# Optimization experiments

Hardware: AMD Instinct MI355X
Metric: run time of the kernel (lower is better)

## Reference

```python
import jax, jax.numpy as jnp
import numpy as np

B, T, S, D = 4, 16, 256, 1024
H, HKV = 16, 4
HD = D // H  # 64
N_IMG = 240  # image tokens; remaining S-N_IMG are agent tokens
LOGIT_CAP = 50.0
EPS = 1e-6


def _build_mask():
    # modality-aware mask: image tokens see only image tokens; agent tokens see all
    m = np.zeros((S, S), dtype=bool)
    m[:N_IMG, :N_IMG] = True
    m[N_IMG:, :] = True
    return jnp.asarray(m)


def _build_rope(s, hd):
    half = hd // 2
    inv_freq = 1.0 / (10000.0 ** (np.arange(half, dtype=np.float32) / half))
    pos = np.arange(s, dtype=np.float32)
    ang = np.outer(pos, inv_freq)  # (S, hd/2)
    return jnp.asarray(np.cos(ang)), jnp.asarray(np.sin(ang))


def setup_inputs() -> dict:
    key = jax.random.key(0)
    ks = jax.random.split(key, 7)
    rope_cos, rope_sin = _build_rope(S, HD)
    sc = 0.02
    return {
        "x": jax.random.normal(ks[0], (B, T, S, D), jnp.float32),
        "attn_mask": _build_mask(),
        "rope_cos": rope_cos,
        "rope_sin": rope_sin,
        "Wq": jax.random.normal(ks[1], (D, H * HD), jnp.float32) * sc,
        "Wk": jax.random.normal(ks[2], (D, HKV * HD), jnp.float32) * sc,
        "Wv": jax.random.normal(ks[3], (D, HKV * HD), jnp.float32) * sc,
        "Wo": jax.random.normal(ks[4], (D, D), jnp.float32) * sc,
        "q_scale": jnp.ones((HD,), jnp.float32),
        "k_scale": jnp.ones((HD,), jnp.float32),
    }


def _rmsnorm(t, scale):
    # RMSNorm over head_dim
    var = jnp.mean(jnp.square(t), axis=-1, keepdims=True)
    return t * jax.lax.rsqrt(var + EPS) * scale


def _rope(t, cos, sin):
    # rotate-half RoPE; t: (N, S, h, hd), cos/sin: (S, hd/2)
    half = t.shape[-1] // 2
    t1, t2 = t[..., :half], t[..., half:]
    c = cos[None, :, None, :]
    s = sin[None, :, None, :]
    return jnp.concatenate([t1 * c - t2 * s, t2 * c + t1 * s], axis=-1)


def reference(x, attn_mask, rope_cos, rope_sin, Wq, Wk, Wv, Wo, q_scale, k_scale):
    b, t, s, d = x.shape
    n = b * t
    xf = x.reshape(n, s, d)
    q = (xf @ Wq).reshape(n, s, H, HD)
    k = (xf @ Wk).reshape(n, s, HKV, HD)
    v = (xf @ Wv).reshape(n, s, HKV, HD)
    # QK-norm then RoPE
    q = _rope(_rmsnorm(q, q_scale), rope_cos, rope_sin)
    k = _rope(_rmsnorm(k, k_scale), rope_cos, rope_sin)
    # GQA: repeat kv heads
    rep = H // HKV
    k = jnp.repeat(k, rep, axis=2)
    v = jnp.repeat(v, rep, axis=2)
    scale = 1.0 / jnp.sqrt(jnp.asarray(HD, x.dtype))
    scores = jnp.einsum('nqhd,nkhd->nhqk', q, k) * scale
    # logit soft-capping
    scores = LOGIT_CAP * jnp.tanh(scores / LOGIT_CAP)
    big_neg = jnp.asarray(jnp.finfo(scores.dtype).min, scores.dtype)
    scores = jnp.where(attn_mask[None, None], scores, big_neg)
    p = jax.nn.softmax(scores, axis=-1)
    out = jnp.einsum('nhqk,nkhd->nqhd', p, v).reshape(n, s, d)
    return (out @ Wo).reshape(b, t, s, d)
```

## Files before the change

kernel.cpp:

```cpp
#include <hip/hip_runtime.h>

typedef __bf16 v8bf __attribute__((ext_vector_type(8)));
typedef __bf16 v4bf __attribute__((ext_vector_type(4)));
typedef float floatx4 __attribute__((ext_vector_type(4)));

#define MFMA16(a, b, c) __builtin_amdgcn_mfma_f32_16x16x32_bf16(a, b, c, 0, 0, 0)
#define GLL16(gp, lp)                                                        \
    __builtin_amdgcn_global_load_lds(                                        \
        (const __attribute__((address_space(1))) void*)(gp),                 \
        (__attribute__((address_space(3))) void*)(lp), 16, 0, 0)

__global__ void cast_x(const float* __restrict__ x, __bf16* __restrict__ xb, int n4) {
    int i = blockIdx.x * blockDim.x + threadIdx.x;
    int stride = gridDim.x * blockDim.x;
    for (; i < n4; i += stride) {
        float4 v = ((const float4*)x)[i];
        v4bf o;
        o[0] = (__bf16)v.x; o[1] = (__bf16)v.y; o[2] = (__bf16)v.z; o[3] = (__bf16)v.w;
        ((v4bf*)xb)[i] = o;
    }
}

__global__ void transW(const float* __restrict__ W0, const float* __restrict__ W1,
                       const float* __restrict__ W2, const float* __restrict__ W3,
                       __bf16* __restrict__ dqkv, __bf16* __restrict__ dwo) {
    __shared__ __bf16 tile[64][65];
    int k0 = blockIdx.x * 64;
    int byy = blockIdx.y;
    bool isO = byy >= 24;
    int c0 = (isO ? byy - 24 : byy) * 64;
    for (int i = threadIdx.x; i < 4096; i += 256) {
        int k = i >> 6, c = i & 63;
        int gc = c0 + c;
        float v;
        if (isO)            v = W3[(k0 + k) * 1024 + gc];
        else if (gc < 1024) v = W0[(k0 + k) * 1024 + gc];
        else if (gc < 1280) v = W1[(k0 + k) * 256 + gc - 1024];
        else                v = W2[(k0 + k) * 256 + gc - 1280];
        tile[c][k] = (__bf16)v;
    }
    __syncthreads();
    __bf16* dst = isO ? dwo : dqkv;
    for (int i = threadIdx.x; i < 4096; i += 256) {
        int c = i >> 6, k = i & 63;
        dst[(c0 + c) * 1024 + k0 + k] = tile[c][k];
    }
}

template <typename OUT>
__global__ __launch_bounds__(256) void gemm_bt(const __bf16* __restrict__ A,
                                               const __bf16* __restrict__ B,
                                               OUT* __restrict__ C, int N) {
    __shared__ __attribute__((aligned(16))) __bf16 smem[16384];
    __bf16* As = smem;
    __bf16* Bs = smem + 8192;
    const int t = threadIdx.x, lane = t & 63, w = t >> 6;
    const int m0 = blockIdx.y * 128, n0 = blockIdx.x * 128;
    const int wm = (w >> 1) * 64, wn = (w & 1) * 64;
    const int rl = lane >> 2;
    const int gl = (lane & 3) ^ ((lane >> 3) & 3);
    const __bf16* pA0 = A + (long)(m0 + w * 16 + rl) * 1024 + gl * 8;
    const __bf16* pA1 = A + (long)(m0 + 64 + w * 16 + rl) * 1024 + gl * 8;
    const __bf16* pB0 = B + (long)(n0 + w * 16 + rl) * 1024 + gl * 8;
    const __bf16* pB1 = B + (long)(n0 + 64 + w * 16 + rl) * 1024 + gl * 8;
    __bf16* lA0 = &As[(w * 16) * 32];
    __bf16* lA1 = &As[(64 + w * 16) * 32];
    __bf16* lB0 = &Bs[(w * 16) * 32];
    __bf16* lB1 = &Bs[(64 + w * 16) * 32];
    const int lr = lane & 15, quad = lane >> 4, m = lane & 15;
    const int ga = ((quad ^ ((lr >> 1) & 3)) * 8);
    floatx4 acc[4][4] = {};
    for (int kk = 0; kk < 1024; kk += 64) {
        __syncthreads();
        GLL16(pA0 + kk, lA0);          GLL16(pA0 + kk + 32, lA0 + 4096);
        GLL16(pA1 + kk, lA1);          GLL16(pA1 + kk + 32, lA1 + 4096);
        GLL16(pB0 + kk, lB0);          GLL16(pB0 + kk + 32, lB0 + 4096);
        GLL16(pB1 + kk, lB1);          GLL16(pB1 + kk + 32, lB1 + 4096);
        __syncthreads();
#pragma unroll
        for (int p = 0; p < 2; ++p) {
            v8bf af[4], bq[4];
#pragma unroll
            for (int i = 0; i < 4; ++i)
                af[i] = *(const v8bf*)(&As[p * 4096 + (wm + i * 16 + lr) * 32 + ga]);
#pragma unroll
            for (int j = 0; j < 4; ++j)
                bq[j] = *(const v8bf*)(&Bs[p * 4096 + (wn + j * 16 + lr) * 32 + ga]);
#pragma unroll
            for (int i = 0; i < 4; ++i)
#pragma unroll
                for (int j = 0; j < 4; ++j)
                    acc[i][j] = MFMA16(af[i], bq[j], acc[i][j]);
        }
    }
    __syncthreads();
    const int row2 = lane >> 2, cb = lane & 3;
    if constexpr (sizeof(OUT) == 2) {
        __bf16* tile = smem + w * (16 * 68);
#pragma unroll
        for (int i = 0; i < 4; ++i) {
#pragma unroll
            for (int j = 0; j < 4; ++j)
#pragma unroll
                for (int r = 0; r < 4; ++r)
                    tile[(quad * 4 + r) * 68 + j * 16 + m] = (__bf16)acc[i][j][r];
            __bf16* dst = (__bf16*)C + (long)(m0 + wm + i * 16 + row2) * N + n0 + wn + cb * 16;
            *(v8bf*)dst = *(const v8bf*)(&tile[row2 * 68 + cb * 16]);
            *(v8bf*)(dst + 8) = *(const v8bf*)(&tile[row2 * 68 + cb * 16 + 8]);
        }
    } else {
        float* tile = (float*)smem + w * (16 * 66);
#pragma unroll
        for (int i = 0; i < 4; ++i) {
#pragma unroll
            for (int j = 0; j < 4; ++j)
#pragma unroll
                for (int r = 0; r < 4; ++r)
                    tile[(quad * 4 + r) * 66 + j * 16 + m] = acc[i][j][r];
            float* dst = (float*)C + (long)(m0 + wm + i * 16 + row2) * N + n0 + wn + cb * 16;
#pragma unroll
            for (int c = 0; c < 4; ++c)
                *(floatx4*)(dst + c * 4) = *(const floatx4*)(&tile[row2 * 66 + cb * 16 + c * 4]);
        }
    }
}

__global__ __launch_bounds__(256) void knorm(const __bf16* __restrict__ qkv,
                                             const float* __restrict__ rc,
                                             const float* __restrict__ rs,
                                             const float* __restrict__ ksc,
                                             __bf16* __restrict__ Kb) {
    int item = blockIdx.x * 4 + (threadIdx.x >> 6);
    int lane = threadIdx.x & 63;
    int row = item >> 2, hk = item & 3;
    int n = row >> 8, s = row & 255;
    float v = (float)qkv[(long)row * 1536 + 1024 + hk * 64 + lane];
    float sq = v * v;
#pragma unroll
    for (int msk = 1; msk < 64; msk <<= 1) sq += __shfl_xor(sq, msk);
    float rr = rsqrtf(sq * (1.f / 64.f) + 1e-6f);
    v = v * rr * ksc[lane];
    float c = rc[s * 32 + (lane & 31)];
    float sn = rs[s * 32 + (lane & 31)];
    float p = __shfl_xor(v, 32);
    v = (lane < 32) ? (v * c - p * sn) : (v * c + p * sn);
    Kb[((long)((n * 4 + hk) * 256 + s) << 6) + lane] = (__bf16)v;
}

__global__ __launch_bounds__(512) void attn_kernel(const __bf16* __restrict__ qkv,
                                                   const __bf16* __restrict__ Kb,
                                                   const float* __restrict__ rc,
                                                   const float* __restrict__ rs,
                                                   const float* __restrict__ qsc,
                                                   __bf16* __restrict__ O) {
    __shared__ __attribute__((aligned(16))) __bf16 KV[256 * 64];
    __shared__ __attribute__((aligned(16))) __bf16 Ps[8][16][40];
    const int bx = blockIdx.x;
    const int n = bx >> 5, h = (bx >> 1) & 15, half = bx & 1, hk = h >> 2;
    const int t = threadIdx.x, lane = t & 63, w = t >> 6;
    const int m = lane & 15, quad = lane >> 4;

    for (int p = 0; p < 4; ++p) {
        int l = t + p * 512;
        int s = l >> 3, cg = l & 7;
        v8bf kv = *(const v8bf*)(Kb + ((long)((n * 4 + hk) * 256 + s) << 6) + cg * 8);
        *(v8bf*)(&KV[s * 64 + ((cg ^ (s & 7)) * 8)]) = kv;
    }
    const int srow = half * 128 + w * 16 + m;
    const __bf16* qp = qkv + (long)(n * 256 + srow) * 1536 + h * 64 + quad * 8;
    v8bf qr0 = *(const v8bf*)(qp);
    v8bf qr1 = *(const v8bf*)(qp + 32);
    float f0[8], f1[8], ss = 0.f;
#pragma unroll
    for (int j = 0; j < 8; ++j) {
        f0[j] = (float)qr0[j]; f1[j] = (float)qr1[j];
        ss += f0[j] * f0[j] + f1[j] * f1[j];
    }
    ss += __shfl_xor(ss, 16);
    ss += __shfl_xor(ss, 32);
    float rr = rsqrtf(ss * (1.f / 64.f) + 1e-6f);
    v8bf qa0, qa1;
#pragma unroll
    for (int j = 0; j < 8; ++j) {
        int hd = quad * 8 + j;
        float t1 = f0[j] * rr * qsc[hd];
        float t2 = f1[j] * rr * qsc[32 + hd];
        float c = rc[srow * 32 + hd], sn = rs[srow * 32 + hd];
        qa0[j] = (__bf16)(t1 * c - t2 * sn);
        qa1[j] = (__bf16)(t2 * c + t1 * sn);
    }
    __syncthreads();

    floatx4 sc[16];
#pragma unroll
    for (int ti = 0; ti < 16; ++ti) {
        int kr = ti * 16 + m;
        v8bf b0 = *(const v8bf*)(&KV[kr * 64 + ((quad ^ (kr & 7)) * 8)]);
        v8bf b1 = *(const v8bf*)(&KV[kr * 64 + (((quad + 4) ^ (kr & 7)) * 8)]);
        floatx4 a = {0.f, 0.f, 0.f, 0.f};
        a = MFMA16(qa0, b0, a);
        a = MFMA16(qa1, b1, a);
        sc[ti] = a;
    }

    const int qbase = half * 128 + w * 16 + quad * 4;
    float sum[4] = {0.f, 0.f, 0.f, 0.f};
#pragma unroll
    for (int ti = 0; ti < 16; ++ti)
#pragma unroll
        for (int r = 0; r < 4; ++r) {
            float v = sc[ti][r];
            float e = __builtin_amdgcn_exp2f(v * 0.0072134752f);
            float capped = 50.f - 100.f * __builtin_amdgcn_rcpf(e + 1.f);
            float p = __builtin_amdgcn_exp2f(capped * 1.44269504f);
            if (ti == 15 && (qbase + r) < 240) p = 0.f;
            sc[ti][r] = p;
            sum[r] += p;
        }
    float inv[4];
#pragma unroll
    for (int r = 0; r < 4; ++r) {
#pragma unroll
        for (int msk = 1; msk < 16; msk <<= 1) sum[r] += __shfl_xor(sum[r], msk);
        inv[r] = __builtin_amdgcn_rcpf(sum[r]);
    }

    __syncthreads();
    for (int p = 0; p < 4; ++p) {
        int l = t + p * 512;
        int s = l >> 3, cg = l & 7;
        v8bf vv = *(const v8bf*)(qkv + (long)(n * 256 + s) * 1536 + 1280 + hk * 64 + cg * 8);
#pragma unroll
        for (int j = 0; j < 8; ++j)
            KV[(cg * 8 + j) * 256 + ((s >> 3) ^ j) * 8 + (s & 7)] = vv[j];
    }
    __syncthreads();

    floatx4 oacc[4] = {};
#pragma unroll
    for (int kc = 0; kc < 8; ++kc) {
#pragma unroll
        for (int ht = 0; ht < 2; ++ht) {
            int ti = kc * 2 + ht;
#pragma unroll
            for (int r = 0; r < 4; ++r)
                Ps[w][quad * 4 + r][ht * 16 + m] = (__bf16)sc[ti][r];
        }
        v8bf pa = *(const v8bf*)(&Ps[w][m][quad * 8]);
#pragma unroll
        for (int ct = 0; ct < 4; ++ct) {
            int hd = ct * 16 + m;
            int sg = kc * 4 + quad;
            v8bf vb = *(const v8bf*)(&KV[hd * 256 + ((sg ^ (hd & 7)) * 8)]);
            oacc[ct] = MFMA16(pa, vb, oacc[ct]);
        }
    }
#pragma unroll
    for (int ct = 0; ct < 4; ++ct)
#pragma unroll
        for (int r = 0; r < 4; ++r) {
            int qrow = half * 128 + w * 16 + quad * 4 + r;
            O[(long)(n * 256 + qrow) * 1024 + h * 64 + ct * 16 + m] =
                (__bf16)(oacc[ct][r] * inv[r]);
        }
}

extern "C" void kernel_launch(void* const* d_in, const int* in_sizes, int n_in,
                              void* d_out, int out_size, void* d_ws, size_t ws_size,
                              hipStream_t stream) {
    const float* x  = (const float*)d_in[0];
    const float* rc = (const float*)d_in[2];
    const float* rs = (const float*)d_in[3];
    const float* Wq = (const float*)d_in[4];
    const float* Wk = (const float*)d_in[5];
    const float* Wv = (const float*)d_in[6];
    const float* Wo = (const float*)d_in[7];
    const float* qs = (const float*)d_in[8];
    const float* ks = (const float*)d_in[9];
    float* out = (float*)d_out;
    char* ws = (char*)d_ws;

    __bf16* x_bf    = (__bf16*)(ws);
    __bf16* WqkvT   = (__bf16*)(ws + (32l << 20));
    __bf16* WoT     = (__bf16*)(ws + (35l << 20));
    __bf16* qkv_bf  = (__bf16*)(ws + (37l << 20));
    __bf16* K_bf    = (__bf16*)(ws + (85l << 20));
    __bf16* attn_bf = (__bf16*)(ws + (93l << 20));

    cast_x<<<4096, 256, 0, stream>>>(x, x_bf, 16777216 / 4);
    transW<<<dim3(16, 40), 256, 0, stream>>>(Wq, Wk, Wv, Wo, WqkvT, WoT);
    gemm_bt<__bf16><<<dim3(12, 128), 256, 0, stream>>>(x_bf, WqkvT, qkv_bf, 1536);
    knorm<<<16384, 256, 0, stream>>>(qkv_bf, rc, rs, ks, K_bf);
    attn_kernel<<<2048, 512, 0, stream>>>(qkv_bf, K_bf, rc, rs, qs, attn_bf);
    gemm_bt<float><<<dim3(8, 128), 256, 0, stream>>>(attn_bf, WoT, out, 1024);
}
```

Measured before the change: 331.1 us.

## Pipeline GEMM with 4-stage async LDS ring, larger tiles and grid swizzle

Rewrites the bf16 GEMM so global-to-LDS loads are issued three k-steps ahead into a 4-slot shared-memory ring, synchronised with explicit vmcnt waits and barriers instead of a full sync per step. Tiles grow to 128x256 or 256x256 with 512 threads, and workgroup ids are remapped so neighbouring blocks share operand tiles in cache. MFMA sections are raised in priority with setprio. The larger LDS footprint and tile size may cut occupancy, and the hand-written wait counts must match the issued loads exactly.

Result: no change. 324.7 us (-1.9%).

```diff
diff --git a/kernel.cpp b/kernel.cpp
--- a/kernel.cpp
+++ b/kernel.cpp
@@ -9,6 +9,8 @@
     __builtin_amdgcn_global_load_lds(                                        \
         (const __attribute__((address_space(1))) void*)(gp),                 \
         (__attribute__((address_space(3))) void*)(lp), 16, 0, 0)
+#define VMW(n) asm volatile("s_waitcnt vmcnt(" #n ")" ::: "memory")
+#define BARRIER() asm volatile("s_barrier" ::: "memory")
 
 __global__ void cast_x(const float* __restrict__ x, __bf16* __restrict__ xb, int n4) {
     int i = blockIdx.x * blockDim.x + threadIdx.x;
@@ -47,58 +49,83 @@
     }
 }
 
-template <typename OUT>
-__global__ __launch_bounds__(256) void gemm_bt(const __bf16* __restrict__ A,
-                                               const __bf16* __restrict__ B,
-                                               OUT* __restrict__ C, int N) {
-    __shared__ __attribute__((aligned(16))) __bf16 smem[16384];
-    __bf16* As = smem;
-    __bf16* Bs = smem + 8192;
+template <int BM, typename OUT>
+__global__ __launch_bounds__(512, 2) void gemm_bt(const __bf16* __restrict__ A,
+                                                  const __bf16* __restrict__ B,
+                                                  OUT* __restrict__ C, int N) {
+    constexpr int MF = BM / 32;
+    constexpr int SLAB = (BM + 256) * 32;
+    __shared__ __attribute__((aligned(16))) __bf16 smem[4 * SLAB];
     const int t = threadIdx.x, lane = t & 63, w = t >> 6;
-    const int m0 = blockIdx.y * 128, n0 = blockIdx.x * 128;
-    const int wm = (w >> 1) * 64, wn = (w & 1) * 64;
+    const int gx = gridDim.x;
+    const int nwg = gx * gridDim.y;
+    const int id = blockIdx.y * gx + blockIdx.x;
+    const int swz = (id & 7) * (nwg >> 3) + (id >> 3);
+    const int m0 = (swz / gx) * BM, n0 = (swz % gx) * 256;
+    const int wm = (w >> 2) * (BM / 2), wn = (w & 3) * 64;
     const int rl = lane >> 2;
     const int gl = (lane & 3) ^ ((lane >> 3) & 3);
-    const __bf16* pA0 = A + (long)(m0 + w * 16 + rl) * 1024 + gl * 8;
-    const __bf16* pA1 = A + (long)(m0 + 64 + w * 16 + rl) * 1024 + gl * 8;
-    const __bf16* pB0 = B + (long)(n0 + w * 16 + rl) * 1024 + gl * 8;
-    const __bf16* pB1 = B + (long)(n0 + 64 + w * 16 + rl) * 1024 + gl * 8;
-    __bf16* lA0 = &As[(w * 16) * 32];
-    __bf16* lA1 = &As[(64 + w * 16) * 32];
-    __bf16* lB0 = &Bs[(w * 16) * 32];
-    __bf16* lB1 = &Bs[(64 + w * 16) * 32];
+    const __bf16* pA = A + (long)(m0 + w * (BM / 8) + rl) * 1024 + gl * 8;
+    const __bf16* pB = B + (long)(n0 + w * 32 + rl) * 1024 + gl * 8;
     const int lr = lane & 15, quad = lane >> 4, m = lane & 15;
     const int ga = ((quad ^ ((lr >> 1) & 3)) * 8);
-    floatx4 acc[4][4] = {};
-    for (int kk = 0; kk < 1024; kk += 64) {
-        __syncthreads();
-        GLL16(pA0 + kk, lA0);          GLL16(pA0 + kk + 32, lA0 + 4096);
-        GLL16(pA1 + kk, lA1);          GLL16(pA1 + kk + 32, lA1 + 4096);
-        GLL16(pB0 + kk, lB0);          GLL16(pB0 + kk + 32, lB0 + 4096);
-        GLL16(pB1 + kk, lB1);          GLL16(pB1 + kk + 32, lB1 + 4096);
-        __syncthreads();
-#pragma unroll
-        for (int p = 0; p < 2; ++p) {
-            v8bf af[4], bq[4];
-#pragma unroll
-            for (int i = 0; i < 4; ++i)
-                af[i] = *(const v8bf*)(&As[p * 4096 + (wm + i * 16 + lr) * 32 + ga]);
+    floatx4 acc[MF][4] = {};
+
+    auto STAGE = [&](int s) {
+        __bf16* base = smem + (s & 3) * SLAB;
+        const __bf16* sa = pA + s * 32;
+        const __bf16* sb = pB + s * 32;
+        if constexpr (BM == 256) {
+            GLL16(sa, base + w * 1024);
+            GLL16(sa + 16 * 1024, base + w * 1024 + 512);
+        } else {
+            GLL16(sa, base + w * 512);
+        }
+        __bf16* bb = base + BM * 32;
+        GLL16(sb, bb + w * 1024);
+        GLL16(sb + 16 * 1024, bb + w * 1024 + 512);
+    };
+    auto COMPUTE = [&](int s) {
+        const __bf16* As_ = smem + (s & 3) * SLAB;
+        const __bf16* Bs_ = As_ + BM * 32;
+        v8bf af[MF], bq[4];
+#pragma unroll
+        for (int i = 0; i < MF; ++i)
+            af[i] = *(const v8bf*)(As_ + (wm + i * 16 + lr) * 32 + ga);
+#pragma unroll
+        for (int j = 0; j < 4; ++j)
+            bq[j] = *(const v8bf*)(Bs_ + (wn + j * 16 + lr) * 32 + ga);
+        __builtin_amdgcn_s_setprio(1);
+#pragma unroll
+        for (int i = 0; i < MF; ++i)
 #pragma unroll
             for (int j = 0; j < 4; ++j)
-                bq[j] = *(const v8bf*)(&Bs[p * 4096 + (wn + j * 16 + lr) * 32 + ga]);
-#pragma unroll
-            for (int i = 0; i < 4; ++i)
-#pragma unroll
-                for (int j = 0; j < 4; ++j)
-                    acc[i][j] = MFMA16(af[i], bq[j], acc[i][j]);
-        }
-    }
-    __syncthreads();
+                acc[i][j] = MFMA16(af[i], bq[j], acc[i][j]);
+        __builtin_amdgcn_s_setprio(0);
+    };
+
+    STAGE(0); STAGE(1); STAGE(2);
+#pragma unroll 1
+    for (int s = 0; s < 29; ++s) {
+        STAGE(s + 3);
+        if constexpr (BM == 256) VMW(12); else VMW(9);
+        BARRIER();
+        COMPUTE(s);
+        BARRIER();
+    }
+    if constexpr (BM == 256) VMW(8); else VMW(6);
+    BARRIER(); COMPUTE(29); BARRIER();
+    if constexpr (BM == 256) VMW(4); else VMW(3);
+    BARRIER(); COMPUTE(30); BARRIER();
+    VMW(0);
+    BARRIER(); COMPUTE(31);
+    __syncthreads();
+
     const int row2 = lane >> 2, cb = lane & 3;
     if constexpr (sizeof(OUT) == 2) {
         __bf16* tile = smem + w * (16 * 68);
 #pragma unroll
-        for (int i = 0; i < 4; ++i) {
+        for (int i = 0; i < MF; ++i) {
 #pragma unroll
             for (int j = 0; j < 4; ++j)
 #pragma unroll
@@ -111,7 +138,7 @@
     } else {
         float* tile = (float*)smem + w * (16 * 66);
 #pragma unroll
-        for (int i = 0; i < 4; ++i) {
+        for (int i = 0; i < MF; ++i) {
 #pragma unroll
             for (int j = 0; j < 4; ++j)
 #pragma unroll
@@ -289,8 +316,8 @@
 
     cast_x<<<4096, 256, 0, stream>>>(x, x_bf, 16777216 / 4);
     transW<<<dim3(16, 40), 256, 0, stream>>>(Wq, Wk, Wv, Wo, WqkvT, WoT);
-    gemm_bt<__bf16><<<dim3(12, 128), 256, 0, stream>>>(x_bf, WqkvT, qkv_bf, 1536);
+    gemm_bt<128, __bf16><<<dim3(6, 128), 512, 0, stream>>>(x_bf, WqkvT, qkv_bf, 1536);
     knorm<<<16384, 256, 0, stream>>>(qkv_bf, rc, rs, ks, K_bf);
     attn_kernel<<<2048, 512, 0, stream>>>(qkv_bf, K_bf, rc, rs, qs, attn_bf);
-    gemm_bt<float><<<dim3(8, 128), 256, 0, stream>>>(attn_bf, WoT, out, 1024);
-}
+    gemm_bt<256, float><<<dim3(4, 64), 512, 0, stream>>>(attn_bf, WoT, out, 1024);
+}
```
